# Kernel optimization log

Hardware: AMD Instinct MI355X
Metric: run time of the kernel (lower is better)

## Reference

```python
import jax, jax.numpy as jnp
import numpy as np

N_NODES = 100000
N_EDGES = 2400000


def setup_inputs() -> dict:
    key = jax.random.key(0)
    ks = jax.random.split(key, 6)
    x = jax.random.normal(ks[0], (N_NODES, 2), dtype=jnp.float32)
    edge_index = jax.random.randint(ks[1], (2, N_EDGES), 0, N_NODES, dtype=jnp.int64)
    # GCNConv weights (glorot-ish scale) and zero biases
    W1 = jax.random.normal(ks[2], (2, 32), dtype=jnp.float32) * (1.0 / np.sqrt(2.0))
    b1 = jnp.zeros((32,), dtype=jnp.float32)
    W2 = jax.random.normal(ks[3], (32, 32), dtype=jnp.float32) * (1.0 / np.sqrt(32.0))
    b2 = jnp.zeros((32,), dtype=jnp.float32)
    W3 = jax.random.normal(ks[4], (32, 1), dtype=jnp.float32) * (1.0 / np.sqrt(32.0))
    b3 = jnp.zeros((1,), dtype=jnp.float32)
    return {"x": x, "edge_index": edge_index, "W1": W1, "b1": b1,
            "W2": W2, "b2": b2, "W3": W3, "b3": b3}


def reference(x, edge_index, W1, b1, W2, b2, W3, b3):
    N = x.shape[0]
    self_loops = jnp.arange(N, dtype=edge_index.dtype)
    src = jnp.concatenate([edge_index[0], self_loops])  # message sources
    dst = jnp.concatenate([edge_index[1], self_loops])  # aggregation targets
    # Symmetric GCN normalization: deg computed at target nodes (PyG gcn_norm)
    deg = jax.ops.segment_sum(jnp.ones_like(dst, dtype=x.dtype), dst, num_segments=N)
    dinv = jnp.where(deg > 0, jax.lax.rsqrt(deg), 0.0)
    norm = (dinv[src] * dinv[dst])[:, None]  # [E+N, 1]

    def gcn_layer(h, W, b):
        h = h @ W                                  # [N, out]
        msg = norm * h[src]                        # gather + scale
        agg = jax.ops.segment_sum(msg, dst, num_segments=N)  # scatter-add
        return agg + b

    h = jax.nn.relu(gcn_layer(x, W1, b1))
    h = jax.nn.relu(gcn_layer(h, W2, b2))
    out = gcn_layer(h, W3, b3)
    return out.reshape(-1)
```

## Files before the change

kernel.cpp:

```cpp
#include <hip/hip_runtime.h>

#define NN 100000
#define NE 2400000
#define NB 391
#define CAP 6912
#define CAP2 7168
#define EPB 4096
#define NBLK2 ((NE + EPB - 1) / EPB)
#define IMASK 0x1FFFF
#define SLACK 131072

__device__ __forceinline__ int wexscan(int v, int lane) {
    int x = v;
#pragma unroll
    for (int off = 1; off < 64; off <<= 1) {
        int t = __shfl_up(x, off, 64);
        x += (lane >= off) ? t : 0;
    }
    return x - v;
}

__global__ __launch_bounds__(512) void k_hist(const int* __restrict__ ei,
        int* __restrict__ bh) {
    __shared__ int hist[NB];
    int tid = threadIdx.x;
    for (int i = tid; i < NB; i += 512) hist[i] = 0;
    __syncthreads();
    int base_e = blockIdx.x * EPB + tid * 8;
    if (base_e + 8 <= NE) {
        int4 da = *(const int4*)(ei + NE + base_e);
        int4 db = *(const int4*)(ei + NE + base_e + 4);
        atomicAdd(&hist[da.x >> 8], 1); atomicAdd(&hist[da.y >> 8], 1);
        atomicAdd(&hist[da.z >> 8], 1); atomicAdd(&hist[da.w >> 8], 1);
        atomicAdd(&hist[db.x >> 8], 1); atomicAdd(&hist[db.y >> 8], 1);
        atomicAdd(&hist[db.z >> 8], 1); atomicAdd(&hist[db.w >> 8], 1);
    }
    __syncthreads();
    for (int i = tid; i < NB; i += 512) bh[blockIdx.x * NB + i] = hist[i];
}

__global__ __launch_bounds__(256) void k_offscan(int* __restrict__ bh,
        int* __restrict__ tot) {
    __shared__ int wsum[4];
    int b = blockIdx.x, tid = threadIdx.x;
    int lane = tid & 63, wid = tid >> 6;
    int carry = 0;
#pragma unroll
    for (int r = 0; r < 3; ++r) {
        int blk = r * 256 + tid;
        int v = (blk < NBLK2) ? bh[blk * NB + b] : 0;
        int ex = wexscan(v, lane);
        if (lane == 63) wsum[wid] = ex + v;
        __syncthreads();
        int woff = 0, rt = 0;
#pragma unroll
        for (int i = 0; i < 4; ++i) {
            woff += (i < wid) ? wsum[i] : 0;
            rt += wsum[i];
        }
        if (blk < NBLK2) bh[blk * NB + b] = b * CAP + carry + woff + ex;
        carry += rt;
        __syncthreads();
    }
    if (tid == 0) tot[b] = carry;
}

__global__ __launch_bounds__(512) void k_scatter2(const int* __restrict__ ei,
        const int* __restrict__ bh, int* __restrict__ binned) {
    __shared__ int hist[NB], lbase[NB], myb[NB];
    __shared__ int stage[EPB];
    __shared__ unsigned short stageb[EPB];
    __shared__ int wsum[8];
    int tid = threadIdx.x;
    for (int i = tid; i < NB; i += 512) {
        hist[i] = 0;
        myb[i] = bh[blockIdx.x * NB + i];
    }
    __syncthreads();
    int base_e = blockIdx.x * EPB + tid * 8;
    int pk[8], bn[8], rk[8];
    if (base_e + 8 <= NE) {
        const int4* s4 = (const int4*)(ei + base_e);
        const int4* d4 = (const int4*)(ei + NE + base_e);
        int4 sa = s4[0], sb = s4[1], da = d4[0], db = d4[1];
        int ss[8] = {sa.x, sa.y, sa.z, sa.w, sb.x, sb.y, sb.z, sb.w};
        int dd[8] = {da.x, da.y, da.z, da.w, db.x, db.y, db.z, db.w};
#pragma unroll
        for (int k = 0; k < 8; ++k) {
            bn[k] = dd[k] >> 8;
            pk[k] = ss[k] | ((dd[k] & 255) << 17);
            rk[k] = atomicAdd(&hist[bn[k]], 1);
        }
    } else {
#pragma unroll
        for (int k = 0; k < 8; ++k) bn[k] = -1;
    }
    __syncthreads();
    int lane = tid & 63, wid = tid >> 6;
    int v = (tid < NB) ? hist[tid] : 0;
    int ex = wexscan(v, lane);
    if (lane == 63) wsum[wid] = ex + v;
    __syncthreads();
    int woff = 0, tot = 0;
#pragma unroll
    for (int i = 0; i < 8; ++i) {
        int s = wsum[i];
        woff += (i < wid) ? s : 0;
        tot += s;
    }
    ex += woff;
    if (tid < NB) lbase[tid] = ex;
    __syncthreads();
#pragma unroll
    for (int k = 0; k < 8; ++k) {
        if (bn[k] >= 0) {
            int slot = lbase[bn[k]] + rk[k];
            stage[slot] = pk[k];
            stageb[slot] = (unsigned short)bn[k];
        }
    }
    __syncthreads();
    for (int j = tid; j < tot; j += 512) {
        int b = stageb[j];
        binned[myb[b] + (j - lbase[b])] = stage[j];
    }
}

__global__ __launch_bounds__(256) void k_csr_count(const int* __restrict__ binned,
        const int* __restrict__ tot, const float* __restrict__ x,
        int* __restrict__ rsp, float* __restrict__ dinv, float2* __restrict__ xs) {
    __shared__ int cnt[256];
    __shared__ int wsum[4];
    int tid = threadIdx.x, b = blockIdx.x;
    int base = b * CAP, n = tot[b];
    cnt[tid] = 0;
    __syncthreads();
    int n4 = n >> 2;
    const int4* b4 = (const int4*)(binned + base);
    for (int j = tid; j < n4; j += 256) {
        int4 w = b4[j];
        atomicAdd(&cnt[(w.x >> 17) & 255], 1);
        atomicAdd(&cnt[(w.y >> 17) & 255], 1);
        atomicAdd(&cnt[(w.z >> 17) & 255], 1);
        atomicAdd(&cnt[(w.w >> 17) & 255], 1);
    }
    for (int j = (n4 << 2) + tid; j < n; j += 256)
        atomicAdd(&cnt[(binned[base + j] >> 17) & 255], 1);
    __syncthreads();
    int deg = cnt[tid];
    int degp = (deg + 3) & ~3;
    int lane = tid & 63, wid = tid >> 6;
    int ex = wexscan(degp, lane);
    if (lane == 63) wsum[wid] = ex + degp;
    __syncthreads();
    int woff = 0;
#pragma unroll
    for (int i = 0; i < 4; ++i) woff += (i < wid) ? wsum[i] : 0;
    ex += woff;
    int node = (b << 8) + tid;
    if (node < NN) {
        rsp[node] = ((b * CAP2 + ex) << 8) | deg;
        float di = rsqrtf((float)(deg + 1));
        dinv[node] = di;
        float2 xv = ((const float2*)x)[node];
        xs[node] = make_float2(di * xv.x, di * xv.y);
    }
    if (node == NN) xs[NN] = make_float2(0.f, 0.f);
}

__global__ __launch_bounds__(256) void k_csr_place(const int* __restrict__ binned,
        const int* __restrict__ tot, const int* __restrict__ rsp,
        const float2* __restrict__ xs, const float* __restrict__ dinv,
        int* __restrict__ csr, float4* __restrict__ At) {
    __shared__ int cur2[256];
    int tid = threadIdx.x, b = blockIdx.x;
    int base = b * CAP, base2 = b * CAP2, n = tot[b];
    int node = (b << 8) + tid;
    int rp = (node < NN) ? rsp[node] : 0;
    cur2[tid] = (node < NN) ? ((rp >> 8) - base2) : 0;
    __syncthreads();
    int n4 = n >> 2;
    const int4* b4 = (const int4*)(binned + base);
    for (int j = tid; j < n4; j += 256) {
        int4 w = b4[j];
        int p0 = atomicAdd(&cur2[(w.x >> 17) & 255], 1); csr[base2 + p0] = w.x & IMASK;
        int p1 = atomicAdd(&cur2[(w.y >> 17) & 255], 1); csr[base2 + p1] = w.y & IMASK;
        int p2 = atomicAdd(&cur2[(w.z >> 17) & 255], 1); csr[base2 + p2] = w.z & IMASK;
        int p3 = atomicAdd(&cur2[(w.w >> 17) & 255], 1); csr[base2 + p3] = w.w & IMASK;
    }
    for (int j = (n4 << 2) + tid; j < n; j += 256) {
        int w = binned[base + j];
        int p = atomicAdd(&cur2[(w >> 17) & 255], 1);
        csr[base2 + p] = w & IMASK;
    }
    __syncthreads();
    if (node == NN) At[NN] = make_float4(0.f, 0.f, 0.f, 0.f);
    if (node < NN) {
        int beg = rp >> 8, deg = rp & 255;
        int degp = (deg + 3) & ~3, nIt = degp >> 2;
        for (int p = deg; p < degp; ++p) csr[beg + p] = NN;
        float ax = 0.f, ay = 0.f;
        const int4* cp = (const int4*)(csr + beg);
        if (nIt > 0) {
            int4 c1 = cp[1];
            int4 c0 = cp[0];
            float2 A0 = xs[c0.x & IMASK], A1 = xs[c0.y & IMASK];
            float2 A2 = xs[c0.z & IMASK], A3 = xs[c0.w & IMASK];
            for (int it = 0; it < nIt; ++it) {
                int4 cn = cp[it + 2];
                float2 B0 = xs[c1.x & IMASK], B1 = xs[c1.y & IMASK];
                float2 B2 = xs[c1.z & IMASK], B3 = xs[c1.w & IMASK];
                ax += (A0.x + A1.x) + (A2.x + A3.x);
                ay += (A0.y + A1.y) + (A2.y + A3.y);
                A0 = B0; A1 = B1; A2 = B2; A3 = B3;
                c1 = cn;
            }
        }
        float di = dinv[node];
        float2 xn = xs[node];
        At[node] = make_float4(di * (ax + xn.x), di * (ay + xn.y), di, 0.f);
    }
}

__global__ __launch_bounds__(256) void k_agg(const float4* __restrict__ At,
        const int* __restrict__ rsp, const int* __restrict__ csr,
        const float* __restrict__ W1, const float* __restrict__ b1,
        const float* __restrict__ W2, const float* __restrict__ b2,
        const float* __restrict__ W3, float* __restrict__ h3) {
    __shared__ float accS[32 * 36];
    __shared__ float diS[32];
    int tid = threadIdx.x;
    if (blockIdx.x == 0 && tid == 0) h3[NN] = 0.f;
    int o = tid & 7, nl = tid >> 3;
    int node = blockIdx.x * 32 + nl;
    int f = tid & 31;

    float4 w0 = *(const float4*)&W1[4 * o];
    float4 w1 = *(const float4*)&W1[32 + 4 * o];
    float4 bb = *(const float4*)&b1[4 * o];

    int r = rsp[node];
    int beg = r >> 8, deg = r & 255;
    int degp = (deg + 3) & ~3, nIt = degp >> 2;
    float4 an = At[node];
    float di = an.z;

    float4 acc;
    {
        float v0 = fmaf(an.y, w1.x, fmaf(an.x, w0.x, bb.x));
        float v1 = fmaf(an.y, w1.y, fmaf(an.x, w0.y, bb.y));
        float v2 = fmaf(an.y, w1.z, fmaf(an.x, w0.z, bb.z));
        float v3 = fmaf(an.y, w1.w, fmaf(an.x, w0.w, bb.w));
        acc.x = di * fmaxf(v0, 0.f);
        acc.y = di * fmaxf(v1, 0.f);
        acc.z = di * fmaxf(v2, 0.f);
        acc.w = di * fmaxf(v3, 0.f);
    }

    auto acc1 = [&](const float4& aa) {
        float v0 = fmaf(aa.y, w1.x, fmaf(aa.x, w0.x, bb.x));
        float v1 = fmaf(aa.y, w1.y, fmaf(aa.x, w0.y, bb.y));
        float v2 = fmaf(aa.y, w1.z, fmaf(aa.x, w0.z, bb.z));
        float v3 = fmaf(aa.y, w1.w, fmaf(aa.x, w0.w, bb.w));
        acc.x = fmaf(aa.z, fmaxf(v0, 0.f), acc.x);
        acc.y = fmaf(aa.z, fmaxf(v1, 0.f), acc.y);
        acc.z = fmaf(aa.z, fmaxf(v2, 0.f), acc.z);
        acc.w = fmaf(aa.z, fmaxf(v3, 0.f), acc.w);
    };

    const int4* cp = (const int4*)(csr + beg);
    {
        int4 c0 = cp[0], c1 = cp[1];
        float4 A0 = At[c0.x & IMASK], A1 = At[c0.y & IMASK];
        float4 A2 = At[c0.z & IMASK], A3 = At[c0.w & IMASK];
        for (int it = 0; it < nIt; ++it) {
            int4 cn = cp[it + 2];
            float4 B0 = At[c1.x & IMASK], B1 = At[c1.y & IMASK];
            float4 B2 = At[c1.z & IMASK], B3 = At[c1.w & IMASK];
            acc1(A0); acc1(A1); acc1(A2); acc1(A3);
            A0 = B0; A1 = B1; A2 = B2; A3 = B3;
            c1 = cn;
        }
    }

    float w2r[32];
#pragma unroll
    for (int k = 0; k < 32; ++k) w2r[k] = W2[k * 32 + f];

    acc.x *= di; acc.y *= di; acc.z *= di; acc.w *= di;
    *(float4*)&accS[nl * 36 + 4 * o] = acc;
    if (o == 0) diS[nl] = di;
    __syncthreads();

    float bf = b2[f], w3f = W3[f];
    int g = tid >> 5;
#pragma unroll
    for (int rr = 0; rr < 4; ++rr) {
        int n = g + 8 * rr;
        const float* arow = &accS[n * 36];
        float sum = bf;
#pragma unroll
        for (int k = 0; k < 32; k += 4) {
            float4 a4 = *(const float4*)&arow[k];
            sum = fmaf(a4.x, w2r[k], sum);
            sum = fmaf(a4.y, w2r[k + 1], sum);
            sum = fmaf(a4.z, w2r[k + 2], sum);
            sum = fmaf(a4.w, w2r[k + 3], sum);
        }
        float h2 = fmaxf(sum, 0.f);
        float v = h2 * w3f;
#pragma unroll
        for (int off = 16; off > 0; off >>= 1) v += __shfl_down(v, off, 32);
        if (f == 0) h3[blockIdx.x * 32 + n] = diS[n] * v;
    }
}

__global__ __launch_bounds__(256) void k_gather_out(const float* __restrict__ hs,
        const int* __restrict__ rsp, const int* __restrict__ csr,
        const float* __restrict__ dinv, const float* __restrict__ bias,
        float* __restrict__ out) {
    int node = blockIdx.x * 256 + threadIdx.x;
    if (node >= NN) return;
    int r = rsp[node];
    int beg = r >> 8, deg = r & 255;
    int degp = (deg + 3) & ~3, nIt = degp >> 2;
    float acc = hs[node];
    const int4* cp = (const int4*)(csr + beg);
    if (nIt > 0) {
        int4 c0 = cp[0], c1 = cp[1];
        float A0 = hs[c0.x & IMASK], A1 = hs[c0.y & IMASK];
        float A2 = hs[c0.z & IMASK], A3 = hs[c0.w & IMASK];
        for (int it = 0; it < nIt; ++it) {
            int4 cn = cp[it + 2];
            float B0 = hs[c1.x & IMASK], B1 = hs[c1.y & IMASK];
            float B2 = hs[c1.z & IMASK], B3 = hs[c1.w & IMASK];
            acc += (A0 + A1) + (A2 + A3);
            A0 = B0; A1 = B1; A2 = B2; A3 = B3;
            c1 = cn;
        }
    }
    out[node] = dinv[node] * acc + bias[0];
}

extern "C" void kernel_launch(void* const* d_in, const int* in_sizes, int n_in,
                              void* d_out, int out_size, void* d_ws, size_t ws_size,
                              hipStream_t stream) {
    const float* x  = (const float*)d_in[0];
    const int*   ei = (const int*)d_in[1];
    const float* W1 = (const float*)d_in[2];
    const float* b1 = (const float*)d_in[3];
    const float* W2 = (const float*)d_in[4];
    const float* b2 = (const float*)d_in[5];
    const float* W3 = (const float*)d_in[6];
    const float* b3 = (const float*)d_in[7];
    float* out = (float*)d_out;

    char* w = (char*)d_ws;
    float4* At    = (float4*)w; w += SLACK * 16;
    float2* xs    = (float2*)w; w += SLACK * 8;
    int*   bh     = (int*)w;    w += NBLK2 * NB * 4;
    int*   tot    = (int*)w;    w += NB * 4;
    int*   rsp    = (int*)w;    w += NN * 4;
    float* dinv   = (float*)w;  w += NN * 4;
    int*   binned = (int*)w;    w += NB * CAP * 4;
    int*   csr    = (int*)w;    w += (NB * CAP2 + 16) * 4;
    float* h3     = (float*)w;  w += SLACK * 4;

    const int G_N = (NN + 255) / 256;
    const int G_A = NN / 32;

    k_hist<<<NBLK2, 512, 0, stream>>>(ei, bh);
    k_offscan<<<NB, 256, 0, stream>>>(bh, tot);
    k_scatter2<<<NBLK2, 512, 0, stream>>>(ei, bh, binned);
    k_csr_count<<<NB, 256, 0, stream>>>(binned, tot, x, rsp, dinv, xs);
    k_csr_place<<<NB, 256, 0, stream>>>(binned, tot, rsp, xs, dinv, csr, At);
    k_agg<<<G_A, 256, 0, stream>>>(At, rsp, csr, W1, b1, W2, b2, W3, h3);
    k_gather_out<<<G_N, 256, 0, stream>>>(h3, rsp, csr, dinv, b3, out);
}
```

Baseline: 168.4 us.

## Replace two-level binned CSR build with global-atomic degree count and placement

```diff
diff --git a/kernel.cpp b/kernel.cpp
--- a/kernel.cpp
+++ b/kernel.cpp
@@ -3,7 +3,6 @@
 #define NN 100000
 #define NE 2400000
 #define NB 391
-#define CAP 6912
 #define CAP2 7168
 #define EPB 4096
 #define NBLK2 ((NE + EPB - 1) / EPB)
@@ -20,206 +19,95 @@
     return x - v;
 }
 
-__global__ __launch_bounds__(512) void k_hist(const int* __restrict__ ei,
-        int* __restrict__ bh) {
-    __shared__ int hist[NB];
-    int tid = threadIdx.x;
-    for (int i = tid; i < NB; i += 512) hist[i] = 0;
-    __syncthreads();
-    int base_e = blockIdx.x * EPB + tid * 8;
+__global__ __launch_bounds__(512) void k_deg(const int* __restrict__ ei,
+        int* __restrict__ deg) {
+    int base_e = blockIdx.x * EPB + threadIdx.x * 8;
     if (base_e + 8 <= NE) {
         int4 da = *(const int4*)(ei + NE + base_e);
         int4 db = *(const int4*)(ei + NE + base_e + 4);
-        atomicAdd(&hist[da.x >> 8], 1); atomicAdd(&hist[da.y >> 8], 1);
-        atomicAdd(&hist[da.z >> 8], 1); atomicAdd(&hist[da.w >> 8], 1);
-        atomicAdd(&hist[db.x >> 8], 1); atomicAdd(&hist[db.y >> 8], 1);
-        atomicAdd(&hist[db.z >> 8], 1); atomicAdd(&hist[db.w >> 8], 1);
-    }
+        atomicAdd(&deg[da.x], 1); atomicAdd(&deg[da.y], 1);
+        atomicAdd(&deg[da.z], 1); atomicAdd(&deg[da.w], 1);
+        atomicAdd(&deg[db.x], 1); atomicAdd(&deg[db.y], 1);
+        atomicAdd(&deg[db.z], 1); atomicAdd(&deg[db.w], 1);
+    }
+}
+
+__global__ __launch_bounds__(256) void k_scan(const float* __restrict__ x,
+        int* __restrict__ deg, int* __restrict__ rsp, float* __restrict__ dinv,
+        float2* __restrict__ xs, int* __restrict__ csr, float4* __restrict__ At) {
+    __shared__ int wsum[4];
+    int tid = threadIdx.x, b = blockIdx.x;
+    int node = (b << 8) + tid;
+    int d = (node < NN) ? deg[node] : 0;
+    int degp = (d + 3) & ~3;
+    int lane = tid & 63, wid = tid >> 6;
+    int ex = wexscan(degp, lane);
+    if (lane == 63) wsum[wid] = ex + degp;
     __syncthreads();
-    for (int i = tid; i < NB; i += 512) bh[blockIdx.x * NB + i] = hist[i];
-}
-
-__global__ __launch_bounds__(256) void k_offscan(int* __restrict__ bh,
-        int* __restrict__ tot) {
-    __shared__ int wsum[4];
-    int b = blockIdx.x, tid = threadIdx.x;
-    int lane = tid & 63, wid = tid >> 6;
-    int carry = 0;
-#pragma unroll
-    for (int r = 0; r < 3; ++r) {
-        int blk = r * 256 + tid;
-        int v = (blk < NBLK2) ? bh[blk * NB + b] : 0;
-        int ex = wexscan(v, lane);
-        if (lane == 63) wsum[wid] = ex + v;
-        __syncthreads();
-        int woff = 0, rt = 0;
-#pragma unroll
-        for (int i = 0; i < 4; ++i) {
-            woff += (i < wid) ? wsum[i] : 0;
-            rt += wsum[i];
-        }
-        if (blk < NBLK2) bh[blk * NB + b] = b * CAP + carry + woff + ex;
-        carry += rt;
-        __syncthreads();
-    }
-    if (tid == 0) tot[b] = carry;
-}
-
-__global__ __launch_bounds__(512) void k_scatter2(const int* __restrict__ ei,
-        const int* __restrict__ bh, int* __restrict__ binned) {
-    __shared__ int hist[NB], lbase[NB], myb[NB];
-    __shared__ int stage[EPB];
-    __shared__ unsigned short stageb[EPB];
-    __shared__ int wsum[8];
-    int tid = threadIdx.x;
-    for (int i = tid; i < NB; i += 512) {
-        hist[i] = 0;
-        myb[i] = bh[blockIdx.x * NB + i];
-    }
-    __syncthreads();
-    int base_e = blockIdx.x * EPB + tid * 8;
-    int pk[8], bn[8], rk[8];
+    int woff = 0;
+#pragma unroll
+    for (int i = 0; i < 4; ++i) woff += (i < wid) ? wsum[i] : 0;
+    ex += woff;
+    if (node < NN) {
+        int beg = b * CAP2 + ex;
+        rsp[node] = (beg << 8) | d;
+        deg[node] = beg;
+        float di = rsqrtf((float)(d + 1));
+        dinv[node] = di;
+        float2 xv = ((const float2*)x)[node];
+        xs[node] = make_float2(di * xv.x, di * xv.y);
+        for (int p = beg + d; p < beg + degp; ++p) csr[p] = NN;
+    }
+    if (node == NN) {
+        xs[NN] = make_float2(0.f, 0.f);
+        At[NN] = make_float4(0.f, 0.f, 0.f, 0.f);
+    }
+}
+
+__global__ __launch_bounds__(512) void k_place(const int* __restrict__ ei,
+        int* __restrict__ cur, int* __restrict__ csr) {
+    int base_e = blockIdx.x * EPB + threadIdx.x * 8;
     if (base_e + 8 <= NE) {
         const int4* s4 = (const int4*)(ei + base_e);
         const int4* d4 = (const int4*)(ei + NE + base_e);
         int4 sa = s4[0], sb = s4[1], da = d4[0], db = d4[1];
         int ss[8] = {sa.x, sa.y, sa.z, sa.w, sb.x, sb.y, sb.z, sb.w};
         int dd[8] = {da.x, da.y, da.z, da.w, db.x, db.y, db.z, db.w};
-#pragma unroll
-        for (int k = 0; k < 8; ++k) {
-            bn[k] = dd[k] >> 8;
-            pk[k] = ss[k] | ((dd[k] & 255) << 17);
-            rk[k] = atomicAdd(&hist[bn[k]], 1);
-        }
-    } else {
-#pragma unroll
-        for (int k = 0; k < 8; ++k) bn[k] = -1;
-    }
-    __syncthreads();
-    int lane = tid & 63, wid = tid >> 6;
-    int v = (tid < NB) ? hist[tid] : 0;
-    int ex = wexscan(v, lane);
-    if (lane == 63) wsum[wid] = ex + v;
-    __syncthreads();
-    int woff = 0, tot = 0;
-#pragma unroll
-    for (int i = 0; i < 8; ++i) {
-        int s = wsum[i];
-        woff += (i < wid) ? s : 0;
-        tot += s;
-    }
-    ex += woff;
-    if (tid < NB) lbase[tid] = ex;
-    __syncthreads();
-#pragma unroll
-    for (int k = 0; k < 8; ++k) {
-        if (bn[k] >= 0) {
-            int slot = lbase[bn[k]] + rk[k];
-            stage[slot] = pk[k];
-            stageb[slot] = (unsigned short)bn[k];
-        }
-    }
-    __syncthreads();
-    for (int j = tid; j < tot; j += 512) {
-        int b = stageb[j];
-        binned[myb[b] + (j - lbase[b])] = stage[j];
-    }
-}
-
-__global__ __launch_bounds__(256) void k_csr_count(const int* __restrict__ binned,
-        const int* __restrict__ tot, const float* __restrict__ x,
-        int* __restrict__ rsp, float* __restrict__ dinv, float2* __restrict__ xs) {
-    __shared__ int cnt[256];
-    __shared__ int wsum[4];
-    int tid = threadIdx.x, b = blockIdx.x;
-    int base = b * CAP, n = tot[b];
-    cnt[tid] = 0;
-    __syncthreads();
-    int n4 = n >> 2;
-    const int4* b4 = (const int4*)(binned + base);
-    for (int j = tid; j < n4; j += 256) {
-        int4 w = b4[j];
-        atomicAdd(&cnt[(w.x >> 17) & 255], 1);
-        atomicAdd(&cnt[(w.y >> 17) & 255], 1);
-        atomicAdd(&cnt[(w.z >> 17) & 255], 1);
-        atomicAdd(&cnt[(w.w >> 17) & 255], 1);
-    }
-    for (int j = (n4 << 2) + tid; j < n; j += 256)
-        atomicAdd(&cnt[(binned[base + j] >> 17) & 255], 1);
-    __syncthreads();
-    int deg = cnt[tid];
-    int degp = (deg + 3) & ~3;
-    int lane = tid & 63, wid = tid >> 6;
-    int ex = wexscan(degp, lane);
-    if (lane == 63) wsum[wid] = ex + degp;
-    __syncthreads();
-    int woff = 0;
-#pragma unroll
-    for (int i = 0; i < 4; ++i) woff += (i < wid) ? wsum[i] : 0;
-    ex += woff;
-    int node = (b << 8) + tid;
-    if (node < NN) {
-        rsp[node] = ((b * CAP2 + ex) << 8) | deg;
-        float di = rsqrtf((float)(deg + 1));
-        dinv[node] = di;
-        float2 xv = ((const float2*)x)[node];
-        xs[node] = make_float2(di * xv.x, di * xv.y);
-    }
-    if (node == NN) xs[NN] = make_float2(0.f, 0.f);
-}
-
-__global__ __launch_bounds__(256) void k_csr_place(const int* __restrict__ binned,
-        const int* __restrict__ tot, const int* __restrict__ rsp,
-        const float2* __restrict__ xs, const float* __restrict__ dinv,
-        int* __restrict__ csr, float4* __restrict__ At) {
-    __shared__ int cur2[256];
-    int tid = threadIdx.x, b = blockIdx.x;
-    int base = b * CAP, base2 = b * CAP2, n = tot[b];
-    int node = (b << 8) + tid;
-    int rp = (node < NN) ? rsp[node] : 0;
-    cur2[tid] = (node < NN) ? ((rp >> 8) - base2) : 0;
-    __syncthreads();
-    int n4 = n >> 2;
-    const int4* b4 = (const int4*)(binned + base);
-    for (int j = tid; j < n4; j += 256) {
-        int4 w = b4[j];
-        int p0 = atomicAdd(&cur2[(w.x >> 17) & 255], 1); csr[base2 + p0] = w.x & IMASK;
-        int p1 = atomicAdd(&cur2[(w.y >> 17) & 255], 1); csr[base2 + p1] = w.y & IMASK;
-        int p2 = atomicAdd(&cur2[(w.z >> 17) & 255], 1); csr[base2 + p2] = w.z & IMASK;
-        int p3 = atomicAdd(&cur2[(w.w >> 17) & 255], 1); csr[base2 + p3] = w.w & IMASK;
-    }
-    for (int j = (n4 << 2) + tid; j < n; j += 256) {
-        int w = binned[base + j];
-        int p = atomicAdd(&cur2[(w >> 17) & 255], 1);
-        csr[base2 + p] = w & IMASK;
-    }
-    __syncthreads();
-    if (node == NN) At[NN] = make_float4(0.f, 0.f, 0.f, 0.f);
-    if (node < NN) {
-        int beg = rp >> 8, deg = rp & 255;
-        int degp = (deg + 3) & ~3, nIt = degp >> 2;
-        for (int p = deg; p < degp; ++p) csr[beg + p] = NN;
-        float ax = 0.f, ay = 0.f;
-        const int4* cp = (const int4*)(csr + beg);
-        if (nIt > 0) {
-            int4 c1 = cp[1];
-            int4 c0 = cp[0];
-            float2 A0 = xs[c0.x & IMASK], A1 = xs[c0.y & IMASK];
-            float2 A2 = xs[c0.z & IMASK], A3 = xs[c0.w & IMASK];
-            for (int it = 0; it < nIt; ++it) {
-                int4 cn = cp[it + 2];
-                float2 B0 = xs[c1.x & IMASK], B1 = xs[c1.y & IMASK];
-                float2 B2 = xs[c1.z & IMASK], B3 = xs[c1.w & IMASK];
-                ax += (A0.x + A1.x) + (A2.x + A3.x);
-                ay += (A0.y + A1.y) + (A2.y + A3.y);
-                A0 = B0; A1 = B1; A2 = B2; A3 = B3;
-                c1 = cn;
-            }
-        }
-        float di = dinv[node];
-        float2 xn = xs[node];
-        At[node] = make_float4(di * (ax + xn.x), di * (ay + xn.y), di, 0.f);
-    }
+        int pp[8];
+#pragma unroll
+        for (int k = 0; k < 8; ++k) pp[k] = atomicAdd(&cur[dd[k]], 1);
+#pragma unroll
+        for (int k = 0; k < 8; ++k) csr[pp[k]] = ss[k];
+    }
+}
+
+__global__ __launch_bounds__(256) void k_At(const int* __restrict__ rsp,
+        const int* __restrict__ csr, const float2* __restrict__ xs,
+        const float* __restrict__ dinv, float4* __restrict__ At) {
+    int node = blockIdx.x * 256 + threadIdx.x;
+    if (node >= NN) return;
+    int rp = rsp[node];
+    int beg = rp >> 8, d = rp & 255;
+    int nIt = ((d + 3) & ~3) >> 2;
+    float ax = 0.f, ay = 0.f;
+    const int4* cp = (const int4*)(csr + beg);
+    if (nIt > 0) {
+        int4 c0 = cp[0], c1 = cp[1];
+        float2 A0 = xs[c0.x & IMASK], A1 = xs[c0.y & IMASK];
+        float2 A2 = xs[c0.z & IMASK], A3 = xs[c0.w & IMASK];
+        for (int it = 0; it < nIt; ++it) {
+            int4 cn = cp[it + 2];
+            float2 B0 = xs[c1.x & IMASK], B1 = xs[c1.y & IMASK];
+            float2 B2 = xs[c1.z & IMASK], B3 = xs[c1.w & IMASK];
+            ax += (A0.x + A1.x) + (A2.x + A3.x);
+            ay += (A0.y + A1.y) + (A2.y + A3.y);
+            A0 = B0; A1 = B1; A2 = B2; A3 = B3;
+            c1 = cn;
+        }
+    }
+    float di = dinv[node];
+    float2 xn = xs[node];
+    At[node] = make_float4(di * (ax + xn.x), di * (ay + xn.y), di, 0.f);
 }
 
 __global__ __launch_bounds__(256) void k_agg(const float4* __restrict__ At,
@@ -241,7 +129,7 @@
 
     int r = rsp[node];
     int beg = r >> 8, deg = r & 255;
-    int degp = (deg + 3) & ~3, nIt = degp >> 2;
+    int nIt = ((deg + 3) & ~3) >> 2;
     float4 an = At[node];
     float di = an.z;
 
@@ -323,7 +211,7 @@
     if (node >= NN) return;
     int r = rsp[node];
     int beg = r >> 8, deg = r & 255;
-    int degp = (deg + 3) & ~3, nIt = degp >> 2;
+    int nIt = ((deg + 3) & ~3) >> 2;
     float acc = hs[node];
     const int4* cp = (const int4*)(csr + beg);
     if (nIt > 0) {
@@ -358,22 +246,20 @@
     char* w = (char*)d_ws;
     float4* At    = (float4*)w; w += SLACK * 16;
     float2* xs    = (float2*)w; w += SLACK * 8;
-    int*   bh     = (int*)w;    w += NBLK2 * NB * 4;
-    int*   tot    = (int*)w;    w += NB * 4;
     int*   rsp    = (int*)w;    w += NN * 4;
+    int*   deg    = (int*)w;    w += NN * 4;
     float* dinv   = (float*)w;  w += NN * 4;
-    int*   binned = (int*)w;    w += NB * CAP * 4;
     int*   csr    = (int*)w;    w += (NB * CAP2 + 16) * 4;
     float* h3     = (float*)w;  w += SLACK * 4;
 
     const int G_N = (NN + 255) / 256;
     const int G_A = NN / 32;
 
-    k_hist<<<NBLK2, 512, 0, stream>>>(ei, bh);
-    k_offscan<<<NB, 256, 0, stream>>>(bh, tot);
-    k_scatter2<<<NBLK2, 512, 0, stream>>>(ei, bh, binned);
-    k_csr_count<<<NB, 256, 0, stream>>>(binned, tot, x, rsp, dinv, xs);
-    k_csr_place<<<NB, 256, 0, stream>>>(binned, tot, rsp, xs, dinv, csr, At);
+    hipMemsetAsync(deg, 0, NN * sizeof(int), stream);
+    k_deg<<<NBLK2, 512, 0, stream>>>(ei, deg);
+    k_scan<<<NB, 256, 0, stream>>>(x, deg, rsp, dinv, xs, csr, At);
+    k_place<<<NBLK2, 512, 0, stream>>>(ei, deg, csr);
+    k_At<<<G_N, 256, 0, stream>>>(rsp, csr, xs, dinv, At);
     k_agg<<<G_A, 256, 0, stream>>>(At, rsp, csr, W1, b1, W2, b2, W3, h3);
     k_gather_out<<<G_N, 256, 0, stream>>>(h3, rsp, csr, dinv, b3, out);
 }
```

Result: slower. 415.1 us (+146.5%).

## Sort nodes by degree within each bin to balance per-thread gather loops

Applied to the files above, without the earlier changes.

```diff
diff --git a/kernel.cpp b/kernel.cpp
--- a/kernel.cpp
+++ b/kernel.cpp
@@ -128,9 +128,11 @@
 
 __global__ __launch_bounds__(256) void k_csr_count(const int* __restrict__ binned,
         const int* __restrict__ tot, const float* __restrict__ x,
-        int* __restrict__ rsp, float* __restrict__ dinv, float2* __restrict__ xs) {
+        int* __restrict__ rsp, float* __restrict__ dinv, float2* __restrict__ xs,
+        int* __restrict__ nmap) {
     __shared__ int cnt[256];
     __shared__ int wsum[4];
+    __shared__ int dhist[256], dbase[256], dcnt[256];
     int tid = threadIdx.x, b = blockIdx.x;
     int base = b * CAP, n = tot[b];
     cnt[tid] = 0;
@@ -166,12 +168,29 @@
         xs[node] = make_float2(di * xv.x, di * xv.y);
     }
     if (node == NN) xs[NN] = make_float2(0.f, 0.f);
+
+    int key = (node < NN) ? ((deg > 250) ? 250 : deg) : 255;
+    dhist[tid] = 0; dcnt[tid] = 0;
+    __syncthreads();
+    atomicAdd(&dhist[key], 1);
+    __syncthreads();
+    int hv = dhist[tid];
+    int hex = wexscan(hv, lane);
+    if (lane == 63) wsum[wid] = hex + hv;
+    __syncthreads();
+    int hoff = 0;
+#pragma unroll
+    for (int i = 0; i < 4; ++i) hoff += (i < wid) ? wsum[i] : 0;
+    dbase[tid] = hex + hoff;
+    __syncthreads();
+    int pos = dbase[key] + atomicAdd(&dcnt[key], 1);
+    nmap[(b << 8) + pos] = (node < NN) ? node : NN;
 }
 
 __global__ __launch_bounds__(256) void k_csr_place(const int* __restrict__ binned,
         const int* __restrict__ tot, const int* __restrict__ rsp,
         const float2* __restrict__ xs, const float* __restrict__ dinv,
-        int* __restrict__ csr, float4* __restrict__ At) {
+        const int* __restrict__ nmap, int* __restrict__ csr, float4* __restrict__ At) {
     __shared__ int cur2[256];
     int tid = threadIdx.x, b = blockIdx.x;
     int base = b * CAP, base2 = b * CAP2, n = tot[b];
@@ -195,15 +214,16 @@
     }
     __syncthreads();
     if (node == NN) At[NN] = make_float4(0.f, 0.f, 0.f, 0.f);
-    if (node < NN) {
-        int beg = rp >> 8, deg = rp & 255;
+    int node2 = nmap[(b << 8) + tid];
+    if (node2 < NN) {
+        int rp2 = rsp[node2];
+        int beg = rp2 >> 8, deg = rp2 & 255;
         int degp = (deg + 3) & ~3, nIt = degp >> 2;
-        for (int p = deg; p < degp; ++p) csr[beg + p] = NN;
+        for (int p = beg + deg; p < beg + degp; ++p) csr[p] = NN;
         float ax = 0.f, ay = 0.f;
         const int4* cp = (const int4*)(csr + beg);
         if (nIt > 0) {
-            int4 c1 = cp[1];
-            int4 c0 = cp[0];
+            int4 c0 = cp[0], c1 = cp[1];
             float2 A0 = xs[c0.x & IMASK], A1 = xs[c0.y & IMASK];
             float2 A2 = xs[c0.z & IMASK], A3 = xs[c0.w & IMASK];
             for (int it = 0; it < nIt; ++it) {
@@ -216,23 +236,25 @@
                 c1 = cn;
             }
         }
-        float di = dinv[node];
-        float2 xn = xs[node];
-        At[node] = make_float4(di * (ax + xn.x), di * (ay + xn.y), di, 0.f);
+        float di = dinv[node2];
+        float2 xn = xs[node2];
+        At[node2] = make_float4(di * (ax + xn.x), di * (ay + xn.y), di, 0.f);
     }
 }
 
 __global__ __launch_bounds__(256) void k_agg(const float4* __restrict__ At,
         const int* __restrict__ rsp, const int* __restrict__ csr,
+        const int* __restrict__ nmap,
         const float* __restrict__ W1, const float* __restrict__ b1,
         const float* __restrict__ W2, const float* __restrict__ b2,
         const float* __restrict__ W3, float* __restrict__ h3) {
     __shared__ float accS[32 * 36];
     __shared__ float diS[32];
+    __shared__ int nodeS[32];
     int tid = threadIdx.x;
     if (blockIdx.x == 0 && tid == 0) h3[NN] = 0.f;
     int o = tid & 7, nl = tid >> 3;
-    int node = blockIdx.x * 32 + nl;
+    int node = nmap[blockIdx.x * 32 + nl];
     int f = tid & 31;
 
     float4 w0 = *(const float4*)&W1[4 * o];
@@ -241,7 +263,7 @@
 
     int r = rsp[node];
     int beg = r >> 8, deg = r & 255;
-    int degp = (deg + 3) & ~3, nIt = degp >> 2;
+    int nIt = ((deg + 3) & ~3) >> 2;
     float4 an = At[node];
     float di = an.z;
 
@@ -289,7 +311,7 @@
 
     acc.x *= di; acc.y *= di; acc.z *= di; acc.w *= di;
     *(float4*)&accS[nl * 36 + 4 * o] = acc;
-    if (o == 0) diS[nl] = di;
+    if (o == 0) { diS[nl] = di; nodeS[nl] = node; }
     __syncthreads();
 
     float bf = b2[f], w3f = W3[f];
@@ -311,19 +333,20 @@
         float v = h2 * w3f;
 #pragma unroll
         for (int off = 16; off > 0; off >>= 1) v += __shfl_down(v, off, 32);
-        if (f == 0) h3[blockIdx.x * 32 + n] = diS[n] * v;
+        if (f == 0) h3[nodeS[n]] = diS[n] * v;
     }
 }
 
 __global__ __launch_bounds__(256) void k_gather_out(const float* __restrict__ hs,
         const int* __restrict__ rsp, const int* __restrict__ csr,
-        const float* __restrict__ dinv, const float* __restrict__ bias,
-        float* __restrict__ out) {
-    int node = blockIdx.x * 256 + threadIdx.x;
+        const int* __restrict__ nmap, const float* __restrict__ dinv,
+        const float* __restrict__ bias, float* __restrict__ out) {
+    int slot = blockIdx.x * 256 + threadIdx.x;
+    int node = nmap[slot];
     if (node >= NN) return;
     int r = rsp[node];
     int beg = r >> 8, deg = r & 255;
-    int degp = (deg + 3) & ~3, nIt = degp >> 2;
+    int nIt = ((deg + 3) & ~3) >> 2;
     float acc = hs[node];
     const int4* cp = (const int4*)(csr + beg);
     if (nIt > 0) {
@@ -361,6 +384,7 @@
     int*   bh     = (int*)w;    w += NBLK2 * NB * 4;
     int*   tot    = (int*)w;    w += NB * 4;
     int*   rsp    = (int*)w;    w += NN * 4;
+    int*   nmap   = (int*)w;    w += NB * 256 * 4;
     float* dinv   = (float*)w;  w += NN * 4;
     int*   binned = (int*)w;    w += NB * CAP * 4;
     int*   csr    = (int*)w;    w += (NB * CAP2 + 16) * 4;
@@ -372,8 +396,8 @@
     k_hist<<<NBLK2, 512, 0, stream>>>(ei, bh);
     k_offscan<<<NB, 256, 0, stream>>>(bh, tot);
     k_scatter2<<<NBLK2, 512, 0, stream>>>(ei, bh, binned);
-    k_csr_count<<<NB, 256, 0, stream>>>(binned, tot, x, rsp, dinv, xs);
-    k_csr_place<<<NB, 256, 0, stream>>>(binned, tot, rsp, xs, dinv, csr, At);
-    k_agg<<<G_A, 256, 0, stream>>>(At, rsp, csr, W1, b1, W2, b2, W3, h3);
-    k_gather_out<<<G_N, 256, 0, stream>>>(h3, rsp, csr, dinv, b3, out);
-}
+    k_csr_count<<<NB, 256, 0, stream>>>(binned, tot, x, rsp, dinv, xs, nmap);
+    k_csr_place<<<NB, 256, 0, stream>>>(binned, tot, rsp, xs, dinv, nmap, csr, At);
+    k_agg<<<G_A, 256, 0, stream>>>(At, rsp, csr, nmap, W1, b1, W2, b2, W3, h3);
+    k_gather_out<<<G_N, 256, 0, stream>>>(h3, rsp, csr, nmap, dinv, b3, out);
+}
```

Result: slower. 175.2 us (+4.0%).

## Fuse CSR count and place via LDS-staged bin, split layer-1 gather into own kernel

Applied to the files above, without the earlier changes.

```diff
diff --git a/kernel.cpp b/kernel.cpp
--- a/kernel.cpp
+++ b/kernel.cpp
@@ -126,26 +126,33 @@
     }
 }
 
-__global__ __launch_bounds__(256) void k_csr_count(const int* __restrict__ binned,
+__global__ __launch_bounds__(256) void k_build(const int* __restrict__ binned,
         const int* __restrict__ tot, const float* __restrict__ x,
-        int* __restrict__ rsp, float* __restrict__ dinv, float2* __restrict__ xs) {
+        int* __restrict__ rsp, float* __restrict__ dinv, float2* __restrict__ xs,
+        int* __restrict__ csr, float4* __restrict__ At) {
+    __shared__ int4 ebin4[CAP / 4];
     __shared__ int cnt[256];
     __shared__ int wsum[4];
+    int* ebin = (int*)ebin4;
     int tid = threadIdx.x, b = blockIdx.x;
-    int base = b * CAP, n = tot[b];
+    int base = b * CAP, base2 = b * CAP2, n = tot[b];
     cnt[tid] = 0;
     __syncthreads();
     int n4 = n >> 2;
     const int4* b4 = (const int4*)(binned + base);
     for (int j = tid; j < n4; j += 256) {
         int4 w = b4[j];
+        ebin4[j] = w;
         atomicAdd(&cnt[(w.x >> 17) & 255], 1);
         atomicAdd(&cnt[(w.y >> 17) & 255], 1);
         atomicAdd(&cnt[(w.z >> 17) & 255], 1);
         atomicAdd(&cnt[(w.w >> 17) & 255], 1);
     }
-    for (int j = (n4 << 2) + tid; j < n; j += 256)
-        atomicAdd(&cnt[(binned[base + j] >> 17) & 255], 1);
+    for (int j = (n4 << 2) + tid; j < n; j += 256) {
+        int w = binned[base + j];
+        ebin[j] = w;
+        atomicAdd(&cnt[(w >> 17) & 255], 1);
+    }
     __syncthreads();
     int deg = cnt[tid];
     int degp = (deg + 3) & ~3;
@@ -159,67 +166,54 @@
     ex += woff;
     int node = (b << 8) + tid;
     if (node < NN) {
-        rsp[node] = ((b * CAP2 + ex) << 8) | deg;
+        rsp[node] = ((base2 + ex) << 8) | deg;
         float di = rsqrtf((float)(deg + 1));
         dinv[node] = di;
         float2 xv = ((const float2*)x)[node];
         xs[node] = make_float2(di * xv.x, di * xv.y);
-    }
-    if (node == NN) xs[NN] = make_float2(0.f, 0.f);
-}
-
-__global__ __launch_bounds__(256) void k_csr_place(const int* __restrict__ binned,
-        const int* __restrict__ tot, const int* __restrict__ rsp,
-        const float2* __restrict__ xs, const float* __restrict__ dinv,
-        int* __restrict__ csr, float4* __restrict__ At) {
-    __shared__ int cur2[256];
-    int tid = threadIdx.x, b = blockIdx.x;
-    int base = b * CAP, base2 = b * CAP2, n = tot[b];
-    int node = (b << 8) + tid;
-    int rp = (node < NN) ? rsp[node] : 0;
-    cur2[tid] = (node < NN) ? ((rp >> 8) - base2) : 0;
-    __syncthreads();
-    int n4 = n >> 2;
-    const int4* b4 = (const int4*)(binned + base);
-    for (int j = tid; j < n4; j += 256) {
-        int4 w = b4[j];
-        int p0 = atomicAdd(&cur2[(w.x >> 17) & 255], 1); csr[base2 + p0] = w.x & IMASK;
-        int p1 = atomicAdd(&cur2[(w.y >> 17) & 255], 1); csr[base2 + p1] = w.y & IMASK;
-        int p2 = atomicAdd(&cur2[(w.z >> 17) & 255], 1); csr[base2 + p2] = w.z & IMASK;
-        int p3 = atomicAdd(&cur2[(w.w >> 17) & 255], 1); csr[base2 + p3] = w.w & IMASK;
-    }
-    for (int j = (n4 << 2) + tid; j < n; j += 256) {
-        int w = binned[base + j];
-        int p = atomicAdd(&cur2[(w >> 17) & 255], 1);
+        int beg = base2 + ex;
+        for (int p = beg + deg; p < beg + degp; ++p) csr[p] = NN;
+    }
+    if (node == NN) {
+        xs[NN] = make_float2(0.f, 0.f);
+        At[NN] = make_float4(0.f, 0.f, 0.f, 0.f);
+    }
+    cnt[tid] = ex;
+    __syncthreads();
+    for (int j = tid; j < n; j += 256) {
+        int w = ebin[j];
+        int p = atomicAdd(&cnt[(w >> 17) & 255], 1);
         csr[base2 + p] = w & IMASK;
     }
-    __syncthreads();
-    if (node == NN) At[NN] = make_float4(0.f, 0.f, 0.f, 0.f);
-    if (node < NN) {
-        int beg = rp >> 8, deg = rp & 255;
-        int degp = (deg + 3) & ~3, nIt = degp >> 2;
-        for (int p = deg; p < degp; ++p) csr[beg + p] = NN;
-        float ax = 0.f, ay = 0.f;
-        const int4* cp = (const int4*)(csr + beg);
-        if (nIt > 0) {
-            int4 c1 = cp[1];
-            int4 c0 = cp[0];
-            float2 A0 = xs[c0.x & IMASK], A1 = xs[c0.y & IMASK];
-            float2 A2 = xs[c0.z & IMASK], A3 = xs[c0.w & IMASK];
-            for (int it = 0; it < nIt; ++it) {
-                int4 cn = cp[it + 2];
-                float2 B0 = xs[c1.x & IMASK], B1 = xs[c1.y & IMASK];
-                float2 B2 = xs[c1.z & IMASK], B3 = xs[c1.w & IMASK];
-                ax += (A0.x + A1.x) + (A2.x + A3.x);
-                ay += (A0.y + A1.y) + (A2.y + A3.y);
-                A0 = B0; A1 = B1; A2 = B2; A3 = B3;
-                c1 = cn;
-            }
-        }
-        float di = dinv[node];
-        float2 xn = xs[node];
-        At[node] = make_float4(di * (ax + xn.x), di * (ay + xn.y), di, 0.f);
-    }
+}
+
+__global__ __launch_bounds__(256) void k_At(const int* __restrict__ rsp,
+        const int* __restrict__ csr, const float2* __restrict__ xs,
+        const float* __restrict__ dinv, float4* __restrict__ At) {
+    int node = blockIdx.x * 256 + threadIdx.x;
+    if (node >= NN) return;
+    int rp = rsp[node];
+    int beg = rp >> 8, d = rp & 255;
+    int nIt = ((d + 3) & ~3) >> 2;
+    float ax = 0.f, ay = 0.f;
+    const int4* cp = (const int4*)(csr + beg);
+    if (nIt > 0) {
+        int4 c0 = cp[0], c1 = cp[1];
+        float2 A0 = xs[c0.x & IMASK], A1 = xs[c0.y & IMASK];
+        float2 A2 = xs[c0.z & IMASK], A3 = xs[c0.w & IMASK];
+        for (int it = 0; it < nIt; ++it) {
+            int4 cn = cp[it + 2];
+            float2 B0 = xs[c1.x & IMASK], B1 = xs[c1.y & IMASK];
+            float2 B2 = xs[c1.z & IMASK], B3 = xs[c1.w & IMASK];
+            ax += (A0.x + A1.x) + (A2.x + A3.x);
+            ay += (A0.y + A1.y) + (A2.y + A3.y);
+            A0 = B0; A1 = B1; A2 = B2; A3 = B3;
+            c1 = cn;
+        }
+    }
+    float di = dinv[node];
+    float2 xn = xs[node];
+    At[node] = make_float4(di * (ax + xn.x), di * (ay + xn.y), di, 0.f);
 }
 
 __global__ __launch_bounds__(256) void k_agg(const float4* __restrict__ At,
@@ -241,7 +235,7 @@
 
     int r = rsp[node];
     int beg = r >> 8, deg = r & 255;
-    int degp = (deg + 3) & ~3, nIt = degp >> 2;
+    int nIt = ((deg + 3) & ~3) >> 2;
     float4 an = At[node];
     float di = an.z;
 
@@ -323,7 +317,7 @@
     if (node >= NN) return;
     int r = rsp[node];
     int beg = r >> 8, deg = r & 255;
-    int degp = (deg + 3) & ~3, nIt = degp >> 2;
+    int nIt = ((deg + 3) & ~3) >> 2;
     float acc = hs[node];
     const int4* cp = (const int4*)(csr + beg);
     if (nIt > 0) {
@@ -372,8 +366,8 @@
     k_hist<<<NBLK2, 512, 0, stream>>>(ei, bh);
     k_offscan<<<NB, 256, 0, stream>>>(bh, tot);
     k_scatter2<<<NBLK2, 512, 0, stream>>>(ei, bh, binned);
-    k_csr_count<<<NB, 256, 0, stream>>>(binned, tot, x, rsp, dinv, xs);
-    k_csr_place<<<NB, 256, 0, stream>>>(binned, tot, rsp, xs, dinv, csr, At);
+    k_build<<<NB, 256, 0, stream>>>(binned, tot, x, rsp, dinv, xs, csr, At);
+    k_At<<<G_N, 256, 0, stream>>>(rsp, csr, xs, dinv, At);
     k_agg<<<G_A, 256, 0, stream>>>(At, rsp, csr, W1, b1, W2, b2, W3, h3);
     k_gather_out<<<G_N, 256, 0, stream>>>(h3, rsp, csr, dinv, b3, out);
 }
```

New measurement: 173.5 us. +3.1%, slower.
